# Kernel tuning notes

Hardware: AMD Instinct MI355X
Metric: run time of the kernel (lower is better)

The kernel has to match this reference:

```python
import jax, jax.numpy as jnp
import numpy as np

EMBED_DIM = 1024
HIDDEN = 128
N_QUERY = 65536
N_PROTO = 512


def setup_inputs() -> dict:
    key = jax.random.key(0)
    k1, k2, k3, k4, k5, k6, k7 = jax.random.split(key, 7)
    d2 = EMBED_DIM * 2
    lim1 = 1.0 / np.sqrt(d2)
    lim2 = 1.0 / np.sqrt(HIDDEN)
    return {
        "query_features": jax.random.normal(k1, (N_QUERY, EMBED_DIM), dtype=jnp.float32),
        "prototypes": jax.random.normal(k2, (N_PROTO, EMBED_DIM), dtype=jnp.float32),
        "distances": jax.random.uniform(k3, (N_QUERY, N_PROTO), dtype=jnp.float32),
        "W1": jax.random.uniform(k4, (d2, HIDDEN), minval=-lim1, maxval=lim1, dtype=jnp.float32),
        "b1": jax.random.uniform(k5, (HIDDEN,), minval=-lim1, maxval=lim1, dtype=jnp.float32),
        "W2": jax.random.uniform(k6, (HIDDEN, 1), minval=-lim2, maxval=lim2, dtype=jnp.float32),
        "b2": jax.random.uniform(k7, (1,), minval=-lim2, maxval=lim2, dtype=jnp.float32),
    }


def reference(query_features, prototypes, distances, W1, b1, W2, b2):
    # Batched version of the per-query loop: argmin -> gather -> concat -> MLP.
    idx = jnp.argmin(distances, axis=1)                      # [N_QUERY]
    closest = prototypes[idx]                                # [N_QUERY, D]
    combined = jnp.concatenate([query_features, closest], axis=-1)  # [N_QUERY, 2D]
    h = jax.nn.relu(combined @ W1 + b1)                      # [N_QUERY, 128]
    out = jax.nn.sigmoid(h @ W2 + b2)                        # [N_QUERY, 1]
    return jnp.squeeze(out, axis=-1)                         # [N_QUERY]
```

## Files before the change

kernel.cpp:

```cpp
#include <hip/hip_runtime.h>
#include <math.h>

#define EMBED 1024
#define HIDDEN 128
#define NPROTO 512

typedef short bf16x8 __attribute__((ext_vector_type(8)));
typedef float f32x4 __attribute__((ext_vector_type(4)));

__device__ __forceinline__ unsigned short f2bf(float x) {
    unsigned u = __builtin_bit_cast(unsigned, x);
    unsigned r = u + 0x7FFFu + ((u >> 16) & 1u);
    return (unsigned short)(r >> 16);
}

__global__ __launch_bounds__(256) void prep_kernel(
    const float* __restrict__ prototypes,
    const float* __restrict__ W1,
    float* __restrict__ proto_h,
    unsigned short* __restrict__ w1t)
{
    int b = blockIdx.x;
    int t = threadIdx.x;
    if (b < 256) {
        int ph = t >> 7, h = t & 127;
        int p = b * 2 + ph;
        const float* pr = prototypes + (size_t)p * EMBED;
        const float* w  = W1 + (size_t)EMBED * HIDDEN + h;
        float acc = 0.f;
        for (int k = 0; k < EMBED; k += 8) {
            #pragma unroll
            for (int j = 0; j < 8; ++j)
                acc += pr[k + j] * w[(size_t)(k + j) * HIDDEN];
        }
        proto_h[(size_t)p * HIDDEN + h] = acc;
    } else {
        int s = (b - 256) * 256 + t;
        int n = s & 127;
        int k0 = (s >> 7) * 8;
        bf16x8 v;
        #pragma unroll
        for (int j = 0; j < 8; ++j)
            v[j] = (short)f2bf(W1[(size_t)(k0 + j) * HIDDEN + n]);
        *(bf16x8*)(w1t + (size_t)n * EMBED + k0) = v;
    }
}

__global__ __launch_bounds__(256, 2) void main_kernel(
    const float* __restrict__ qf,
    const float* __restrict__ dist,
    const float* __restrict__ b1,
    const float* __restrict__ W2,
    const float* __restrict__ b2,
    const float* __restrict__ proto_h,
    const unsigned short* __restrict__ w1t,
    float* __restrict__ out)
{
    __shared__ int s_idx[4][32];

    const int t = threadIdx.x;
    const int wave = t >> 6, lane = t & 63;
    const int quad = lane >> 4, tid16 = lane & 15;
    const int q0 = blockIdx.x * 128 + wave * 32;

    const float* abase = qf + (size_t)(q0 + tid16) * EMBED + quad * 8;
    const unsigned short* bbase = w1t + (size_t)tid16 * EMBED + quad * 8;

    float4 aA[2][2], aB[2][2];
    #pragma unroll
    for (int mi = 0; mi < 2; ++mi) {
        const float* p = abase + (size_t)(mi * 16) * EMBED;
        aA[mi][0] = *(const float4*)(p);
        aA[mi][1] = *(const float4*)(p + 4);
        aB[mi][0] = *(const float4*)(p + 32);
        aB[mi][1] = *(const float4*)(p + 36);
    }

    for (int i = 0; i < 32; i += 4) {
        float4 v0[4], v1[4];
        #pragma unroll
        for (int j = 0; j < 4; ++j) {
            const float* dr = dist + (size_t)(q0 + i + j) * NPROTO;
            v0[j] = ((const float4*)dr)[lane];
            v1[j] = ((const float4*)dr)[lane + 64];
        }
        #pragma unroll
        for (int j = 0; j < 4; ++j) {
            float bv = v0[j].x; int bi = lane * 4;
            if (v0[j].y < bv) { bv = v0[j].y; bi = lane * 4 + 1; }
            if (v0[j].z < bv) { bv = v0[j].z; bi = lane * 4 + 2; }
            if (v0[j].w < bv) { bv = v0[j].w; bi = lane * 4 + 3; }
            int c = 256 + lane * 4;
            if (v1[j].x < bv) { bv = v1[j].x; bi = c; }
            if (v1[j].y < bv) { bv = v1[j].y; bi = c + 1; }
            if (v1[j].z < bv) { bv = v1[j].z; bi = c + 2; }
            if (v1[j].w < bv) { bv = v1[j].w; bi = c + 3; }
            #pragma unroll
            for (int s = 1; s < 64; s <<= 1) {
                float ov = __shfl_xor(bv, s);
                int   oi = __shfl_xor(bi, s);
                if (ov < bv || (ov == bv && oi < bi)) { bv = ov; bi = oi; }
            }
            if (lane == 0) s_idx[wave][i + j] = bi;
        }
    }

    f32x4 acc[2][8];
    #pragma unroll
    for (int mi = 0; mi < 2; ++mi)
        #pragma unroll
        for (int ni = 0; ni < 8; ++ni)
            acc[mi][ni] = (f32x4){0.f, 0.f, 0.f, 0.f};

#define LOAD_A(dst, kk)                                              \
    do {                                                             \
        _Pragma("unroll")                                            \
        for (int mi = 0; mi < 2; ++mi) {                             \
            const float* p = abase + (size_t)(mi * 16) * EMBED + (kk) * 32; \
            dst[mi][0] = *(const float4*)(p);                        \
            dst[mi][1] = *(const float4*)(p + 4);                    \
        }                                                            \
    } while (0)

#define CVT_A(af, src)                                               \
    do {                                                             \
        _Pragma("unroll")                                            \
        for (int mi = 0; mi < 2; ++mi) {                             \
            af[mi][0] = (short)f2bf(src[mi][0].x);                   \
            af[mi][1] = (short)f2bf(src[mi][0].y);                   \
            af[mi][2] = (short)f2bf(src[mi][0].z);                   \
            af[mi][3] = (short)f2bf(src[mi][0].w);                   \
            af[mi][4] = (short)f2bf(src[mi][1].x);                   \
            af[mi][5] = (short)f2bf(src[mi][1].y);                   \
            af[mi][6] = (short)f2bf(src[mi][1].z);                   \
            af[mi][7] = (short)f2bf(src[mi][1].w);                   \
        }                                                            \
    } while (0)

    for (int k = 0; k < 32; k += 2) {
        {
            bf16x8 bfr[8];
            #pragma unroll
            for (int ni = 0; ni < 8; ++ni)
                bfr[ni] = *(const bf16x8*)(bbase + (size_t)(ni * 16) * EMBED + k * 32);
            bf16x8 af[2];
            CVT_A(af, aA);
            if (k + 2 < 32) LOAD_A(aA, k + 2);
            #pragma unroll
            for (int mi = 0; mi < 2; ++mi)
                #pragma unroll
                for (int ni = 0; ni < 8; ++ni)
                    acc[mi][ni] = __builtin_amdgcn_mfma_f32_16x16x32_bf16(
                        af[mi], bfr[ni], acc[mi][ni], 0, 0, 0);
        }
        {
            bf16x8 bfr[8];
            #pragma unroll
            for (int ni = 0; ni < 8; ++ni)
                bfr[ni] = *(const bf16x8*)(bbase + (size_t)(ni * 16) * EMBED + (k + 1) * 32);
            bf16x8 af[2];
            CVT_A(af, aB);
            if (k + 3 < 32) LOAD_A(aB, k + 3);
            #pragma unroll
            for (int mi = 0; mi < 2; ++mi)
                #pragma unroll
                for (int ni = 0; ni < 8; ++ni)
                    acc[mi][ni] = __builtin_amdgcn_mfma_f32_16x16x32_bf16(
                        af[mi], bfr[ni], acc[mi][ni], 0, 0, 0);
        }
    }
#undef LOAD_A
#undef CVT_A

    float b1v[8], w2v[8];
    #pragma unroll
    for (int ni = 0; ni < 8; ++ni) {
        b1v[ni] = b1[ni * 16 + tid16];
        w2v[ni] = W2[ni * 16 + tid16];
    }
    const float b2v = b2[0];
    #pragma unroll
    for (int mi = 0; mi < 2; ++mi) {
        #pragma unroll
        for (int r = 0; r < 4; ++r) {
            int m = mi * 16 + quad * 4 + r;
            const float* ph = proto_h + (size_t)s_idx[wave][m] * HIDDEN + tid16;
            float sum = 0.f;
            #pragma unroll
            for (int ni = 0; ni < 8; ++ni) {
                float v = acc[mi][ni][r] + b1v[ni] + ph[ni * 16];
                sum += fmaxf(v, 0.f) * w2v[ni];
            }
            #pragma unroll
            for (int s = 1; s < 16; s <<= 1) sum += __shfl_xor(sum, s);
            if (tid16 == 0) out[q0 + m] = 1.f / (1.f + expf(-(sum + b2v)));
        }
    }
}

extern "C" void kernel_launch(void* const* d_in, const int* in_sizes, int n_in,
                              void* d_out, int out_size, void* d_ws, size_t ws_size,
                              hipStream_t stream) {
    const float* qf    = (const float*)d_in[0];
    const float* proto = (const float*)d_in[1];
    const float* dist  = (const float*)d_in[2];
    const float* W1    = (const float*)d_in[3];
    const float* b1    = (const float*)d_in[4];
    const float* W2    = (const float*)d_in[5];
    const float* b2    = (const float*)d_in[6];
    float* out = (float*)d_out;

    float* proto_h = (float*)d_ws;
    unsigned short* w1t = (unsigned short*)((char*)d_ws + 512 * 128 * 4);

    prep_kernel<<<320, 256, 0, stream>>>(proto, W1, proto_h, w1t);

    int nq = in_sizes[0] / EMBED;
    main_kernel<<<nq / 128, 256, 0, stream>>>(qf, dist, b1, W2, b2, proto_h, w1t, out);
}
```

Baseline: 529.4 us.

## Stage query tiles in LDS via async global_load_lds with register-resident W1

Restructures the main kernel to 512-thread blocks over 64 queries. Each wave keeps its 16-column slice of W1 resident in registers, and query rows are staged into double-buffered, swizzled LDS with global_load_lds, then converted to bf16 with a cheaper packed round. The hidden-dimension reduction moves to a cross-wave LDS step, and the prototype projection in the prep kernel is split across two K halves for more parallelism. The aim is to overlap streaming of the 256MB query matrix with MFMA work and stop re-reading W1 per K step. The trade-offs are heavy register use (32 bf16x8 for B), extra barriers, and rounding that changes from round-to-nearest-even to round-half-up.

```diff
diff --git a/kernel.cpp b/kernel.cpp
--- a/kernel.cpp
+++ b/kernel.cpp
@@ -7,12 +7,22 @@
 
 typedef short bf16x8 __attribute__((ext_vector_type(8)));
 typedef float f32x4 __attribute__((ext_vector_type(4)));
+typedef unsigned int u32x4 __attribute__((ext_vector_type(4)));
 
 __device__ __forceinline__ unsigned short f2bf(float x) {
     unsigned u = __builtin_bit_cast(unsigned, x);
-    unsigned r = u + 0x7FFFu + ((u >> 16) & 1u);
-    return (unsigned short)(r >> 16);
-}
+    return (unsigned short)((u + 0x8000u) >> 16);
+}
+__device__ __forceinline__ unsigned pk2(float a, float b) {
+    unsigned ua = __builtin_bit_cast(unsigned, a) + 0x8000u;
+    unsigned ub = __builtin_bit_cast(unsigned, b) + 0x8000u;
+    return (ua >> 16) | (ub & 0xFFFF0000u);
+}
+
+#define GLL16(gptr, lptr)                                                \
+    __builtin_amdgcn_global_load_lds(                                    \
+        (const __attribute__((address_space(1))) void*)(gptr),           \
+        (__attribute__((address_space(3))) void*)(lptr), 16, 0, 0)
 
 __global__ __launch_bounds__(256) void prep_kernel(
     const float* __restrict__ prototypes,
@@ -22,20 +32,22 @@
 {
     int b = blockIdx.x;
     int t = threadIdx.x;
-    if (b < 256) {
-        int ph = t >> 7, h = t & 127;
-        int p = b * 2 + ph;
-        const float* pr = prototypes + (size_t)p * EMBED;
-        const float* w  = W1 + (size_t)EMBED * HIDDEN + h;
+    if (b < 512) {
+        __shared__ float s_part[128];
+        int ks = t >> 7, h = t & 127;
+        const float* pr = prototypes + (size_t)b * EMBED + ks * 512;
+        const float* w  = W1 + (size_t)(EMBED + ks * 512) * HIDDEN + h;
         float acc = 0.f;
-        for (int k = 0; k < EMBED; k += 8) {
+        for (int k = 0; k < 512; k += 8) {
             #pragma unroll
             for (int j = 0; j < 8; ++j)
                 acc += pr[k + j] * w[(size_t)(k + j) * HIDDEN];
         }
-        proto_h[(size_t)p * HIDDEN + h] = acc;
+        if (ks) s_part[h] = acc;
+        __syncthreads();
+        if (!ks) proto_h[(size_t)b * HIDDEN + h] = acc + s_part[h];
     } else {
-        int s = (b - 256) * 256 + t;
+        int s = (b - 512) * 256 + t;
         int n = s & 127;
         int k0 = (s >> 7) * 8;
         bf16x8 v;
@@ -46,7 +58,7 @@
     }
 }
 
-__global__ __launch_bounds__(256, 2) void main_kernel(
+__global__ __launch_bounds__(512, 2) void main_kernel(
     const float* __restrict__ qf,
     const float* __restrict__ dist,
     const float* __restrict__ b1,
@@ -56,146 +68,144 @@
     const unsigned short* __restrict__ w1t,
     float* __restrict__ out)
 {
-    __shared__ int s_idx[4][32];
+    __shared__ __align__(16) char lds_a[2][32768];
+    __shared__ int s_idx[64];
+    __shared__ float s_red[64][8];
 
     const int t = threadIdx.x;
     const int wave = t >> 6, lane = t & 63;
     const int quad = lane >> 4, tid16 = lane & 15;
-    const int q0 = blockIdx.x * 128 + wave * 32;
-
-    const float* abase = qf + (size_t)(q0 + tid16) * EMBED + quad * 8;
-    const unsigned short* bbase = w1t + (size_t)tid16 * EMBED + quad * 8;
-
-    float4 aA[2][2], aB[2][2];
+    const int q0 = blockIdx.x * 64;
+
+    bf16x8 B[32];
+    {
+        const unsigned short* wb = w1t + (size_t)(wave * 16 + tid16) * EMBED + quad * 8;
+        #pragma unroll
+        for (int ks = 0; ks < 32; ++ks)
+            B[ks] = *(const bf16x8*)(wb + ks * 32);
+    }
+
+    const char* gsrc[4];
+    {
+        int rl = wave * 8 + (lane >> 5);
+        int j16 = (lane & 31) * 16;
+        #pragma unroll
+        for (int i = 0; i < 4; ++i) {
+            int r = rl + 2 * i;
+            int swz = ((r & 3) << 5) | (((r >> 3) & 1) << 4);
+            gsrc[i] = (const char*)qf + (size_t)(q0 + r) * 4096 + (j16 ^ swz);
+        }
+    }
+
+#define STAGE(s) do {                                                    \
+        char* lb_ = &lds_a[(s) & 1][wave * 4096];                        \
+        _Pragma("unroll")                                                \
+        for (int i_ = 0; i_ < 4; ++i_)                                   \
+            GLL16(gsrc[i_] + (s) * 512, lb_ + i_ * 1024);                \
+    } while (0)
+
+    STAGE(0);
+    STAGE(1);
+
+    {
+        const int q0w = q0 + wave * 8;
+        for (int i = 0; i < 8; i += 4) {
+            float4 v0[4], v1[4];
+            #pragma unroll
+            for (int j = 0; j < 4; ++j) {
+                const float* dr = dist + (size_t)(q0w + i + j) * NPROTO;
+                v0[j] = ((const float4*)dr)[lane];
+                v1[j] = ((const float4*)dr)[lane + 64];
+            }
+            #pragma unroll
+            for (int j = 0; j < 4; ++j) {
+                float bv = v0[j].x; int bi = lane * 4;
+                if (v0[j].y < bv) { bv = v0[j].y; bi = lane * 4 + 1; }
+                if (v0[j].z < bv) { bv = v0[j].z; bi = lane * 4 + 2; }
+                if (v0[j].w < bv) { bv = v0[j].w; bi = lane * 4 + 3; }
+                int c = 256 + lane * 4;
+                if (v1[j].x < bv) { bv = v1[j].x; bi = c; }
+                if (v1[j].y < bv) { bv = v1[j].y; bi = c + 1; }
+                if (v1[j].z < bv) { bv = v1[j].z; bi = c + 2; }
+                if (v1[j].w < bv) { bv = v1[j].w; bi = c + 3; }
+                #pragma unroll
+                for (int s = 1; s < 64; s <<= 1) {
+                    float ov = __shfl_xor(bv, s);
+                    int   oi = __shfl_xor(bi, s);
+                    if (ov < bv || (ov == bv && oi < bi)) { bv = ov; bi = oi; }
+                }
+                if (lane == 0) s_idx[wave * 8 + i + j] = bi;
+            }
+        }
+    }
+
+    f32x4 acc[4];
     #pragma unroll
-    for (int mi = 0; mi < 2; ++mi) {
-        const float* p = abase + (size_t)(mi * 16) * EMBED;
-        aA[mi][0] = *(const float4*)(p);
-        aA[mi][1] = *(const float4*)(p + 4);
-        aB[mi][0] = *(const float4*)(p + 32);
-        aB[mi][1] = *(const float4*)(p + 36);
-    }
-
-    for (int i = 0; i < 32; i += 4) {
-        float4 v0[4], v1[4];
-        #pragma unroll
-        for (int j = 0; j < 4; ++j) {
-            const float* dr = dist + (size_t)(q0 + i + j) * NPROTO;
-            v0[j] = ((const float4*)dr)[lane];
-            v1[j] = ((const float4*)dr)[lane + 64];
-        }
-        #pragma unroll
-        for (int j = 0; j < 4; ++j) {
-            float bv = v0[j].x; int bi = lane * 4;
-            if (v0[j].y < bv) { bv = v0[j].y; bi = lane * 4 + 1; }
-            if (v0[j].z < bv) { bv = v0[j].z; bi = lane * 4 + 2; }
-            if (v0[j].w < bv) { bv = v0[j].w; bi = lane * 4 + 3; }
-            int c = 256 + lane * 4;
-            if (v1[j].x < bv) { bv = v1[j].x; bi = c; }
-            if (v1[j].y < bv) { bv = v1[j].y; bi = c + 1; }
-            if (v1[j].z < bv) { bv = v1[j].z; bi = c + 2; }
-            if (v1[j].w < bv) { bv = v1[j].w; bi = c + 3; }
-            #pragma unroll
-            for (int s = 1; s < 64; s <<= 1) {
-                float ov = __shfl_xor(bv, s);
-                int   oi = __shfl_xor(bi, s);
-                if (ov < bv || (ov == bv && oi < bi)) { bv = ov; bi = oi; }
-            }
-            if (lane == 0) s_idx[wave][i + j] = bi;
-        }
-    }
-
-    f32x4 acc[2][8];
+    for (int mi = 0; mi < 4; ++mi)
+        acc[mi] = (f32x4){0.f, 0.f, 0.f, 0.f};
+
+    const int abase = tid16 * 512 + ((quad * 32) ^ ((tid16 & 3) << 5))
+                    + (((tid16 >> 3) & 1) << 4);
+
+#define WAITB(N) do {                                                    \
+        asm volatile("s_waitcnt vmcnt(" #N ")\n\ts_barrier" ::: "memory"); \
+        __builtin_amdgcn_sched_barrier(0);                               \
+    } while (0)
+#define BAR() __builtin_amdgcn_s_barrier()
+
+#define COMPUTE(s) do {                                                  \
+        const char* La = lds_a[(s) & 1];                                 \
+        _Pragma("unroll")                                                \
+        for (int kk = 0; kk < 4; ++kk) {                                 \
+            _Pragma("unroll")                                            \
+            for (int mi = 0; mi < 4; ++mi) {                             \
+                int o = abase + mi * 8192 + kk * 128;                    \
+                float4 lo = *(const float4*)(La + o);                    \
+                float4 hi = *(const float4*)(La + (o ^ 16));             \
+                u32x4 p_;                                                \
+                p_.x = pk2(lo.x, lo.y); p_.y = pk2(lo.z, lo.w);          \
+                p_.z = pk2(hi.x, hi.y); p_.w = pk2(hi.z, hi.w);          \
+                bf16x8 af = __builtin_bit_cast(bf16x8, p_);              \
+                acc[mi] = __builtin_amdgcn_mfma_f32_16x16x32_bf16(       \
+                    af, B[(s) * 4 + kk], acc[mi], 0, 0, 0);              \
+            }                                                            \
+        }                                                                \
+    } while (0)
+
+    WAITB(4); COMPUTE(0); BAR(); STAGE(2);
+    WAITB(4); COMPUTE(1); BAR(); STAGE(3);
+    WAITB(4); COMPUTE(2); BAR(); STAGE(4);
+    WAITB(4); COMPUTE(3); BAR(); STAGE(5);
+    WAITB(4); COMPUTE(4); BAR(); STAGE(6);
+    WAITB(4); COMPUTE(5); BAR(); STAGE(7);
+    WAITB(4); COMPUTE(6);
+    WAITB(0); COMPUTE(7);
+
+    const int n = wave * 16 + tid16;
+    const float b1v = b1[n];
+    const float w2v = W2[n];
     #pragma unroll
-    for (int mi = 0; mi < 2; ++mi)
-        #pragma unroll
-        for (int ni = 0; ni < 8; ++ni)
-            acc[mi][ni] = (f32x4){0.f, 0.f, 0.f, 0.f};
-
-#define LOAD_A(dst, kk)                                              \
-    do {                                                             \
-        _Pragma("unroll")                                            \
-        for (int mi = 0; mi < 2; ++mi) {                             \
-            const float* p = abase + (size_t)(mi * 16) * EMBED + (kk) * 32; \
-            dst[mi][0] = *(const float4*)(p);                        \
-            dst[mi][1] = *(const float4*)(p + 4);                    \
-        }                                                            \
-    } while (0)
-
-#define CVT_A(af, src)                                               \
-    do {                                                             \
-        _Pragma("unroll")                                            \
-        for (int mi = 0; mi < 2; ++mi) {                             \
-            af[mi][0] = (short)f2bf(src[mi][0].x);                   \
-            af[mi][1] = (short)f2bf(src[mi][0].y);                   \
-            af[mi][2] = (short)f2bf(src[mi][0].z);                   \
-            af[mi][3] = (short)f2bf(src[mi][0].w);                   \
-            af[mi][4] = (short)f2bf(src[mi][1].x);                   \
-            af[mi][5] = (short)f2bf(src[mi][1].y);                   \
-            af[mi][6] = (short)f2bf(src[mi][1].z);                   \
-            af[mi][7] = (short)f2bf(src[mi][1].w);                   \
-        }                                                            \
-    } while (0)
-
-    for (int k = 0; k < 32; k += 2) {
-        {
-            bf16x8 bfr[8];
-            #pragma unroll
-            for (int ni = 0; ni < 8; ++ni)
-                bfr[ni] = *(const bf16x8*)(bbase + (size_t)(ni * 16) * EMBED + k * 32);
-            bf16x8 af[2];
-            CVT_A(af, aA);
-            if (k + 2 < 32) LOAD_A(aA, k + 2);
-            #pragma unroll
-            for (int mi = 0; mi < 2; ++mi)
-                #pragma unroll
-                for (int ni = 0; ni < 8; ++ni)
-                    acc[mi][ni] = __builtin_amdgcn_mfma_f32_16x16x32_bf16(
-                        af[mi], bfr[ni], acc[mi][ni], 0, 0, 0);
-        }
-        {
-            bf16x8 bfr[8];
-            #pragma unroll
-            for (int ni = 0; ni < 8; ++ni)
-                bfr[ni] = *(const bf16x8*)(bbase + (size_t)(ni * 16) * EMBED + (k + 1) * 32);
-            bf16x8 af[2];
-            CVT_A(af, aB);
-            if (k + 3 < 32) LOAD_A(aB, k + 3);
-            #pragma unroll
-            for (int mi = 0; mi < 2; ++mi)
-                #pragma unroll
-                for (int ni = 0; ni < 8; ++ni)
-                    acc[mi][ni] = __builtin_amdgcn_mfma_f32_16x16x32_bf16(
-                        af[mi], bfr[ni], acc[mi][ni], 0, 0, 0);
-        }
-    }
-#undef LOAD_A
-#undef CVT_A
-
-    float b1v[8], w2v[8];
-    #pragma unroll
-    for (int ni = 0; ni < 8; ++ni) {
-        b1v[ni] = b1[ni * 16 + tid16];
-        w2v[ni] = W2[ni * 16 + tid16];
-    }
-    const float b2v = b2[0];
-    #pragma unroll
-    for (int mi = 0; mi < 2; ++mi) {
+    for (int mi = 0; mi < 4; ++mi) {
         #pragma unroll
         for (int r = 0; r < 4; ++r) {
             int m = mi * 16 + quad * 4 + r;
-            const float* ph = proto_h + (size_t)s_idx[wave][m] * HIDDEN + tid16;
-            float sum = 0.f;
-            #pragma unroll
-            for (int ni = 0; ni < 8; ++ni) {
-                float v = acc[mi][ni][r] + b1v[ni] + ph[ni * 16];
-                sum += fmaxf(v, 0.f) * w2v[ni];
-            }
+            float v = acc[mi][r] + b1v + proto_h[(size_t)s_idx[m] * HIDDEN + n];
+            float sum = fmaxf(v, 0.f) * w2v;
             #pragma unroll
             for (int s = 1; s < 16; s <<= 1) sum += __shfl_xor(sum, s);
-            if (tid16 == 0) out[q0 + m] = 1.f / (1.f + expf(-(sum + b2v)));
-        }
-    }
+            if (tid16 == 0) s_red[m][wave] = sum;
+        }
+    }
+    __syncthreads();
+    if (t < 64) {
+        float s = s_red[t][0] + s_red[t][1] + s_red[t][2] + s_red[t][3]
+                + s_red[t][4] + s_red[t][5] + s_red[t][6] + s_red[t][7] + b2[0];
+        out[q0 + t] = 1.f / (1.f + expf(-s));
+    }
+#undef STAGE
+#undef WAITB
+#undef BAR
+#undef COMPUTE
 }
 
 extern "C" void kernel_launch(void* const* d_in, const int* in_sizes, int n_in,
@@ -213,8 +223,8 @@
     float* proto_h = (float*)d_ws;
     unsigned short* w1t = (unsigned short*)((char*)d_ws + 512 * 128 * 4);
 
-    prep_kernel<<<320, 256, 0, stream>>>(proto, W1, proto_h, w1t);
+    prep_kernel<<<576, 256, 0, stream>>>(proto, W1, proto_h, w1t);
 
     int nq = in_sizes[0] / EMBED;
-    main_kernel<<<nq / 128, 256, 0, stream>>>(qf, dist, b1, W2, b2, proto_h, w1t, out);
-}
+    main_kernel<<<nq / 64, 512, 0, stream>>>(qf, dist, b1, W2, b2, proto_h, w1t, out);
+}
```

Result: faster. 508.0 us (-4.0%).
